# Optimization experiments

Hardware: AMD Instinct MI355X
Metric: run time of the kernel (lower is better)

## Reference

```python
import jax, jax.numpy as jnp
import numpy as np
import math

B, S, D, H, NB = 32, 512, 512, 8, 2
DK = D // H
DF = 4 * D
EPS = 1e-8


def layer_norm(x, gamma, beta):
    # Matches torch: unbiased std (ddof=1), divide by (std + eps)
    mean = jnp.mean(x, axis=-1, keepdims=True)
    std = jnp.sqrt(jnp.var(x, axis=-1, keepdims=True, ddof=1))
    return gamma * (x - mean) / (std + EPS) + beta


def block(x, wq, bq, wk, bk, wv, bv, wr, br, ga, ba, wc1, bc1, wc2, bc2, gf, bf):
    # --- attention with ReLU-gated Q/K/V ---
    Q = jax.nn.relu(x @ wq.T + bq)  # [B,S,D]
    K = jax.nn.relu(x @ wk.T + bk)
    V = jax.nn.relu(x @ wv.T + bv)
    # chunk along last dim -> heads; head-major stacking is equivalent to this reshape
    Qh = Q.reshape(B, S, H, DK)
    Kh = K.reshape(B, S, H, DK)
    Vh = V.reshape(B, S, H, DK)
    scores = jnp.einsum('bqhd,bkhd->bhqk', Qh, Kh) / math.sqrt(DK)
    w = jax.nn.softmax(scores, axis=-1)
    out = jnp.einsum('bhqk,bkhd->bqhd', w, Vh).reshape(B, S, D)
    out = out + jax.nn.relu(x @ wr.T + br)
    out = layer_norm(out, ga, ba)
    # --- conv1d (kernel=1) feed-forward ---
    h = jax.nn.relu(out @ wc1.T + bc1)  # [B,S,4D]
    y = h @ wc2.T + bc2                 # [B,S,D]
    y = layer_norm(y + out, gf, bf)
    return y


def setup_inputs() -> dict:
    key = jax.random.key(0)
    ks = jax.random.split(key, 8)
    std = 0.01
    inp = {
        'x': jax.random.normal(ks[0], (B, S, D), jnp.float32),
        'wq': jax.random.normal(ks[1], (NB, D, D), jnp.float32) * std,
        'bq': jnp.zeros((NB, D), jnp.float32),
        'wk': jax.random.normal(ks[2], (NB, D, D), jnp.float32) * std,
        'bk': jnp.zeros((NB, D), jnp.float32),
        'wv': jax.random.normal(ks[3], (NB, D, D), jnp.float32) * std,
        'bv': jnp.zeros((NB, D), jnp.float32),
        'wr': jax.random.normal(ks[4], (NB, D, D), jnp.float32) * std,
        'br': jnp.zeros((NB, D), jnp.float32),
        'g_attn': jnp.ones((NB, D), jnp.float32),
        'b_attn': jnp.zeros((NB, D), jnp.float32),
        'wc1': jax.random.normal(ks[5], (NB, DF, D), jnp.float32) * (1.0 / math.sqrt(D)),
        'bc1': jnp.zeros((NB, DF), jnp.float32),
        'wc2': jax.random.normal(ks[6], (NB, D, DF), jnp.float32) * (1.0 / math.sqrt(DF)),
        'bc2': jnp.zeros((NB, D), jnp.float32),
        'g_ffn': jnp.ones((NB, D), jnp.float32),
        'b_ffn': jnp.zeros((NB, D), jnp.float32),
    }
    return inp


def reference(x, wq, bq, wk, bk, wv, bv, wr, br, g_attn, b_attn,
              wc1, bc1, wc2, bc2, g_ffn, b_ffn):
    enc = x
    for i in range(NB):
        enc = block(enc, wq[i], bq[i], wk[i], bk[i], wv[i], bv[i], wr[i], br[i],
                    g_attn[i], b_attn[i], wc1[i], bc1[i], wc2[i], bc2[i],
                    g_ffn[i], b_ffn[i])
    return enc
```

## Files before the change

kernel.cpp:

```cpp
#include <hip/hip_runtime.h>

typedef unsigned short u16;
typedef __bf16 bf16x8 __attribute__((ext_vector_type(8)));
typedef float f32x4 __attribute__((ext_vector_type(4)));
typedef unsigned short ushort8 __attribute__((ext_vector_type(8)));

__device__ __forceinline__ void gload_lds16(const void* g, void* l) {
  __builtin_amdgcn_global_load_lds(
      (const __attribute__((address_space(1))) void*)g,
      (__attribute__((address_space(3))) void*)l, 16, 0, 0);
}

__device__ __forceinline__ u16 f2bf(float f) {
  unsigned int u = __builtin_bit_cast(unsigned int, f);
  u = (u + 0x7fffu + ((u >> 16) & 1u)) >> 16;
  return (u16)u;
}
__device__ __forceinline__ u16 f2bf_trunc(float f) {
  return (u16)(__builtin_bit_cast(unsigned int, f) >> 16);
}
__device__ __forceinline__ float bf2f(u16 u) {
  unsigned int v = (unsigned int)u << 16;
  return __builtin_bit_cast(float, v);
}

__global__ void castk(const float* __restrict__ in, u16* __restrict__ out, int n,
                      float scale) {
  size_t i = ((size_t)blockIdx.x * 256 + threadIdx.x) * 8;
  if (i >= (size_t)n) return;
  const float4* p = (const float4*)(in + i);
  float4 a = p[0], b = p[1];
  ushort8 o;
  o[0] = f2bf(a.x * scale); o[1] = f2bf(a.y * scale);
  o[2] = f2bf(a.z * scale); o[3] = f2bf(a.w * scale);
  o[4] = f2bf(b.x * scale); o[5] = f2bf(b.y * scale);
  o[6] = f2bf(b.z * scale); o[7] = f2bf(b.w * scale);
  *(ushort8*)(out + i) = o;
}

__global__ void biasg(const float* __restrict__ b0, const float* __restrict__ b1,
                      const float* __restrict__ b2, const float* __restrict__ b3,
                      float* __restrict__ out) {
  int idx = blockIdx.x * 256 + threadIdx.x;
  int i = idx >> 11, j = (idx >> 9) & 3, c = idx & 511;
  const float* src = (j == 0) ? b0 : (j == 1) ? b1 : (j == 2) ? b2 : b3;
  float v = src[i * 512 + c];
  out[idx] = (j == 0) ? v * 0.125f : v;
}

template<int BN, int RELU, int WVT>
__global__ __launch_bounds__(512, 4)
void gemm128(const u16* __restrict__ A, const u16* __restrict__ W,
             const float* __restrict__ bias, u16* __restrict__ C,
             u16* __restrict__ VT, int M, int N, int K)
{
  constexpr int CN   = BN / 4;
  constexpr int NF   = CN / 16;
  constexpr int ATSZ = 128 * 64;
  constexpr int BTSZ = BN * 64;
  constexpr int BLB  = BN / 128;
  constexpr int VC   = 1 + BLB;
  constexpr int PSZ  = 3 * (ATSZ + BTSZ);
  constexpr int ESZ  = 128 * BN * 2;
  constexpr int LSZ  = (PSZ > ESZ) ? PSZ : ESZ;

  __shared__ char lds[LSZ];

  const int tid = threadIdx.x, w = tid >> 6, l = tid & 63;
  const int l15 = l & 15, lh = l >> 4;
  const int nbn = N / BN;
  const int p = blockIdx.x;
  const int bm = (p & 7) * 16 + (p >> 3) / nbn;
  const int bn = (p >> 3) % nbn;
  const int wm = w >> 2, wn = w & 3;
  const int NT = K >> 5;

  const int srow = l >> 2;
  const int scol = ((l & 3) ^ ((l >> 3) & 3)) << 3;
  const u16* aS = A + (size_t)(bm * 128 + w * 16 + srow) * K + scol;
  const u16* bS[BLB];
#pragma unroll
  for (int j = 0; j < BLB; ++j)
    bS[j] = W + (size_t)(bn * BN + (w * BLB + j) * 16 + srow) * K + scol;

  auto stage = [&](int t) {
    const int bsel = t % 3;
    gload_lds16(aS + t * 32, lds + bsel * (ATSZ + BTSZ) + w * 1024);
#pragma unroll
    for (int j = 0; j < BLB; ++j)
      gload_lds16(bS[j] + t * 32,
                  lds + bsel * (ATSZ + BTSZ) + ATSZ + (w * BLB + j) * 1024);
  };

  f32x4 acc[4][NF] = {};
  const int sw = ((l15 >> 1) & 3) << 4;

  stage(0); stage(1);
  for (int u = 0; u < NT; ++u) {
    if (u + 1 < NT) asm volatile("s_waitcnt vmcnt(%0)" :: "i"(VC) : "memory");
    else            asm volatile("s_waitcnt vmcnt(0)" ::: "memory");
    __builtin_amdgcn_s_barrier();
    __builtin_amdgcn_sched_barrier(0);
    if (u + 2 < NT) stage(u + 2);

    const char* Ab = lds + (u % 3) * (ATSZ + BTSZ);
    const char* Bb = Ab + ATSZ;
    bf16x8 a[4], b[NF];
#pragma unroll
    for (int mf = 0; mf < 4; ++mf) {
      int row = wm * 64 + mf * 16 + l15;
      a[mf] = *(const bf16x8*)(Ab + row * 64 + ((lh << 4) ^ sw));
    }
#pragma unroll
    for (int nf = 0; nf < NF; ++nf) {
      int row = wn * CN + nf * 16 + l15;
      b[nf] = *(const bf16x8*)(Bb + row * 64 + ((lh << 4) ^ sw));
    }
    __builtin_amdgcn_s_setprio(1);
#pragma unroll
    for (int mf = 0; mf < 4; ++mf)
#pragma unroll
      for (int nf = 0; nf < NF; ++nf)
        acc[mf][nf] = __builtin_amdgcn_mfma_f32_16x16x32_bf16(a[mf], b[nf], acc[mf][nf], 0, 0, 0);
    __builtin_amdgcn_s_setprio(0);
  }

  __syncthreads();
  char* Ct = (char*)lds;
  const int rowL = wm * 64 + (lh << 2);
  const int colL = wn * CN + l15;
  const bool dovt = WVT && (bn == 4 || bn == 5);
  float bv[NF];
#pragma unroll
  for (int nf = 0; nf < NF; ++nf) bv[nf] = bias[bn * BN + colL + nf * 16];

  if (!dovt) {
#pragma unroll
    for (int mf = 0; mf < 4; ++mf)
#pragma unroll
      for (int nf = 0; nf < NF; ++nf)
#pragma unroll
        for (int r = 0; r < 4; ++r) {
          float v = acc[mf][nf][r] + bv[nf];
          if (RELU) v = fmaxf(v, 0.f);
          int m = rowL + mf * 16 + r, n = colL + nf * 16;
          *(u16*)(Ct + m * (BN * 2) + ((n * 2) ^ ((m & 7) << 4))) = f2bf(v);
        }
    __syncthreads();
    constexpr int TPR = (BN * 2) / 16;
    constexpr int RPP = 512 / TPR;
#pragma unroll
    for (int pass = 0; pass < 128 / RPP; ++pass) {
      int row = pass * RPP + tid / TPR;
      int c16 = tid % TPR;
      bf16x8 vv = *(const bf16x8*)(Ct + row * (BN * 2) + ((c16 * 16) ^ ((row & 7) << 4)));
      *(bf16x8*)(&C[(size_t)(bm * 128 + row) * N + bn * BN + c16 * 8]) = vv;
    }
  } else {
#pragma unroll
    for (int mf = 0; mf < 4; ++mf)
#pragma unroll
      for (int nf = 0; nf < NF; ++nf)
#pragma unroll
        for (int r = 0; r < 4; ++r) {
          float v = acc[mf][nf][r] + bv[nf];
          if (RELU) v = fmaxf(v, 0.f);
          int m = rowL + mf * 16 + r, d = colL + nf * 16;
          *(u16*)(Ct + d * 256 + ((m * 2) ^ ((d & 7) << 4))) = f2bf(v);
        }
    __syncthreads();
    const int batch = bm >> 2;
#pragma unroll
    for (int pass = 0; pass < 8; ++pass) {
      int dL = pass * 32 + (tid >> 4);
      int m16 = tid & 15;
      bf16x8 vv = *(const bf16x8*)(Ct + dL * 256 + ((m16 * 16) ^ ((dL & 7) << 4)));
      int head = (bn - 4) * 4 + (dL >> 6);
      int vtr = (batch * 8 + head) * 64 + (dL & 63);
      *(bf16x8*)(&VT[(size_t)vtr * 512 + (bm & 3) * 128 + m16 * 8]) = vv;
    }
  }
}

__global__ __launch_bounds__(256, 2)
void attn_kernel(const u16* __restrict__ qkvr, const u16* __restrict__ VT,
                 u16* __restrict__ F)
{
  const int D4 = 2048;
  __shared__ u16 Qs[128 * 64];
  __shared__ u16 Ks[2][64 * 64];
  __shared__ u16 Vs[2][64 * 64];
  __shared__ u16 Ps[128 * 64];

  const int tid = threadIdx.x, w = tid >> 6, l = tid & 63;
  const int bh = blockIdx.x & 255, qt = blockIdx.x >> 8;
  const int b = bh >> 3, h = bh & 7;
  const int lr = l >> 3, lc = ((l & 7) ^ lr) << 3;
  const int l15 = l & 15, lh = l >> 4;

  const u16* qG = qkvr + (size_t)(b * 512 + qt * 128) * D4 + h * 64 + lc;
#pragma unroll
  for (int i = 0; i < 4; ++i) {
    int c = w * 4 + i;
    gload_lds16(qG + (size_t)(c * 8 + lr) * D4, &Qs[c * 512]);
  }

  const u16* kG = qkvr + (size_t)(b * 512) * D4 + 512 + h * 64 + lc;
  const u16* vG = VT + (size_t)(bh * 64) * 512 + lc;

  auto stageKV = [&](int kt) {
    const int bsel = kt & 1;
#pragma unroll
    for (int i = 0; i < 2; ++i) {
      int c = w * 2 + i;
      gload_lds16(kG + (size_t)(kt * 64 + c * 8 + lr) * D4, &Ks[bsel][c * 512]);
      gload_lds16(vG + (size_t)(c * 8 + lr) * 512 + kt * 64, &Vs[bsel][c * 512]);
    }
  };
  stageKV(0);

  f32x4 o_acc[2][4] = {};
  float psum[2][4] = {};

  for (int kt = 0; kt < 8; ++kt) {
    __syncthreads();
    if (kt < 7) stageKV(kt + 1);
    const char* Kb = (const char*)Ks[kt & 1];
    const char* Vb = (const char*)Vs[kt & 1];

    f32x4 sacc[2][4] = {};
#pragma unroll
    for (int kk = 0; kk < 2; ++kk) {
      bf16x8 qa[2];
#pragma unroll
      for (int qq = 0; qq < 2; ++qq) {
        int qrow = w * 32 + qq * 16 + l15;
        qa[qq] = *(const bf16x8*)((const char*)Qs + qrow * 128 +
                  ((kk * 64 + (lh << 4)) ^ ((qrow & 7) << 4)));
      }
#pragma unroll
      for (int ni = 0; ni < 4; ++ni) {
        int krow = ni * 16 + l15;
        bf16x8 kb = *(const bf16x8*)(Kb + krow * 128 +
                    ((kk * 64 + (lh << 4)) ^ ((krow & 7) << 4)));
#pragma unroll
        for (int qq = 0; qq < 2; ++qq)
          sacc[qq][ni] = __builtin_amdgcn_mfma_f32_16x16x32_bf16(qa[qq], kb, sacc[qq][ni], 0, 0, 0);
      }
    }

#pragma unroll
    for (int qq = 0; qq < 2; ++qq)
#pragma unroll
      for (int r = 0; r < 4; ++r) {
        float p0 = __expf(sacc[qq][0][r]);
        float p1 = __expf(sacc[qq][1][r]);
        float p2 = __expf(sacc[qq][2][r]);
        float p3 = __expf(sacc[qq][3][r]);
        psum[qq][r] += (p0 + p1) + (p2 + p3);
        int q = w * 32 + qq * 16 + (lh << 2) + r;
        int sw = (q & 7) << 4;
        int col = l15 * 2;
        char* pb = (char*)Ps + q * 128;
        *(u16*)(pb + ((0  + col) ^ sw)) = f2bf_trunc(p0);
        *(u16*)(pb + ((32 + col) ^ sw)) = f2bf_trunc(p1);
        *(u16*)(pb + ((64 + col) ^ sw)) = f2bf_trunc(p2);
        *(u16*)(pb + ((96 + col) ^ sw)) = f2bf_trunc(p3);
      }

#pragma unroll
    for (int kk = 0; kk < 2; ++kk) {
      bf16x8 pa[2];
#pragma unroll
      for (int qq = 0; qq < 2; ++qq) {
        int qrow = w * 32 + qq * 16 + l15;
        pa[qq] = *(const bf16x8*)((const char*)Ps + qrow * 128 +
                  ((kk * 64 + (lh << 4)) ^ ((qrow & 7) << 4)));
      }
#pragma unroll
      for (int ni = 0; ni < 4; ++ni) {
        int d = ni * 16 + l15;
        bf16x8 vb = *(const bf16x8*)(Vb + d * 128 +
                    ((kk * 64 + (lh << 4)) ^ ((d & 7) << 4)));
#pragma unroll
        for (int qq = 0; qq < 2; ++qq)
          o_acc[qq][ni] = __builtin_amdgcn_mfma_f32_16x16x32_bf16(pa[qq], vb, o_acc[qq][ni], 0, 0, 0);
      }
    }
  }

  float lsum[2][4];
#pragma unroll
  for (int qq = 0; qq < 2; ++qq)
#pragma unroll
    for (int r = 0; r < 4; ++r) {
      float t = psum[qq][r];
#pragma unroll
      for (int m = 1; m < 16; m <<= 1) t += __shfl_xor(t, m);
      lsum[qq][r] = 1.f / t;
    }

#pragma unroll
  for (int qq = 0; qq < 2; ++qq)
#pragma unroll
    for (int ni = 0; ni < 4; ++ni) {
      int d = ni * 16 + l15;
#pragma unroll
      for (int r = 0; r < 4; ++r) {
        float v = o_acc[qq][ni][r] * lsum[qq][r];
        int q = w * 32 + qq * 16 + (lh << 2) + r;
        *(u16*)((char*)Ps + q * 128 + ((d * 2) ^ ((q & 7) << 4))) = f2bf(v);
      }
    }
  __syncthreads();
  const u16* Rbase = qkvr + (size_t)(b * 512 + qt * 128) * D4 + 1536 + h * 64;
  u16* Fbase = F + (size_t)(b * 512 + qt * 128) * 512 + h * 64;
#pragma unroll
  for (int pass = 0; pass < 4; ++pass) {
    int row = pass * 32 + (tid >> 3), c8 = tid & 7;
    ushort8 lv = *(const ushort8*)((char*)Ps + row * 128 + ((c8 * 16) ^ ((row & 7) << 4)));
    ushort8 rv = *(const ushort8*)(Rbase + (size_t)row * D4 + c8 * 8);
    ushort8 o;
#pragma unroll
    for (int j = 0; j < 8; ++j) o[j] = f2bf(bf2f(lv[j]) + bf2f(rv[j]));
    *(ushort8*)(Fbase + (size_t)row * 512 + c8 * 8) = o;
  }
}

template<int HAS_RES, int OUT_F32>
__global__ __launch_bounds__(256)
void ln_bf(const u16* __restrict__ in, const u16* __restrict__ res,
           const float* __restrict__ gamma, const float* __restrict__ beta,
           u16* __restrict__ outb, float* __restrict__ outf)
{
  const int l = threadIdx.x & 63;
  const size_t row = (size_t)blockIdx.x * 4 + (threadIdx.x >> 6);
  ushort8 iv = *(const ushort8*)(in + row * 512 + l * 8);
  float x[8];
#pragma unroll
  for (int j = 0; j < 8; ++j) x[j] = bf2f(iv[j]);
  if (HAS_RES) {
    ushort8 rv = *(const ushort8*)(res + row * 512 + l * 8);
#pragma unroll
    for (int j = 0; j < 8; ++j) x[j] += bf2f(rv[j]);
  }
  float s = 0.f, ss = 0.f;
#pragma unroll
  for (int j = 0; j < 8; ++j) { s += x[j]; ss += x[j] * x[j]; }
#pragma unroll
  for (int m = 1; m < 64; m <<= 1) { s += __shfl_xor(s, m); ss += __shfl_xor(ss, m); }
  float mean = s * (1.f / 512.f);
  float var = fmaxf((ss - 512.f * mean * mean) * (1.f / 511.f), 0.f);
  float inv = 1.f / (sqrtf(var) + 1e-8f);
  const float4* g4 = (const float4*)gamma;
  const float4* b4 = (const float4*)beta;
  float4 g0 = g4[l * 2], g1 = g4[l * 2 + 1];
  float4 b0 = b4[l * 2], b1 = b4[l * 2 + 1];
  float gg[8] = {g0.x, g0.y, g0.z, g0.w, g1.x, g1.y, g1.z, g1.w};
  float bb[8] = {b0.x, b0.y, b0.z, b0.w, b1.x, b1.y, b1.z, b1.w};
  float y[8];
#pragma unroll
  for (int j = 0; j < 8; ++j) y[j] = gg[j] * (x[j] - mean) * inv + bb[j];
  ushort8 o;
#pragma unroll
  for (int j = 0; j < 8; ++j) o[j] = f2bf(y[j]);
  *(ushort8*)(outb + row * 512 + l * 8) = o;
  if (OUT_F32) {
    float4* o4 = (float4*)(outf + row * 512);
    o4[l * 2]     = make_float4(y[0], y[1], y[2], y[3]);
    o4[l * 2 + 1] = make_float4(y[4], y[5], y[6], y[7]);
  }
}

extern "C" void kernel_launch(void* const* d_in, const int* in_sizes, int n_in,
                              void* d_out, int out_size, void* d_ws, size_t ws_size,
                              hipStream_t stream)
{
  const int B = 32, S = 512, D = 512, NB = 2, DF = 2048;
  const int M = B * S;

  const float* x   = (const float*)d_in[0];
  const float* wsrc[4] = {(const float*)d_in[1], (const float*)d_in[3],
                          (const float*)d_in[5], (const float*)d_in[7]};
  const float* ga  = (const float*)d_in[9];
  const float* ba  = (const float*)d_in[10];
  const float* wc1 = (const float*)d_in[11];
  const float* bc1 = (const float*)d_in[12];
  const float* wc2 = (const float*)d_in[13];
  const float* bc2 = (const float*)d_in[14];
  const float* gf  = (const float*)d_in[15];
  const float* bfp = (const float*)d_in[16];

  char* ws = (char*)d_ws;
  u16*   curb = (u16*)(ws + 0);
  u16*   qkvr = (u16*)(ws + 16777216);
  u16*   F    = (u16*)(ws + 83886080);
  u16*   Hg   = (u16*)(ws + 100663296);
  u16*   VT   = (u16*)(ws + 117440512);
  u16*   w4b  = (u16*)(ws + 134217728);
  u16*   wc1b = (u16*)(ws + 138412032);
  u16*   wc2b = (u16*)(ws + 142606336);
  float* b4   = (float*)(ws + 146800640);
  u16*   Ih   = qkvr;
  u16*   Y    = F;

  castk<<<M * D / 2048, 256, 0, stream>>>(x, curb, M * D, 1.0f);
  for (int i = 0; i < NB; ++i)
    for (int j = 0; j < 4; ++j)
      castk<<<128, 256, 0, stream>>>(wsrc[j] + (size_t)i * 262144,
                                     w4b + (size_t)i * 1048576 + j * 262144, 262144,
                                     (j == 0) ? 0.125f : 1.0f);
  biasg<<<16, 256, 0, stream>>>((const float*)d_in[2], (const float*)d_in[4],
                                (const float*)d_in[6], (const float*)d_in[8], b4);
  castk<<<NB * DF * D / 2048, 256, 0, stream>>>(wc1, wc1b, NB * DF * D, 1.0f);
  castk<<<NB * DF * D / 2048, 256, 0, stream>>>(wc2, wc2b, NB * DF * D, 1.0f);

  for (int i = 0; i < NB; ++i) {
    const size_t wfo = (size_t)i * DF * D;
    gemm128<256, 1, 1><<<1024, 512, 0, stream>>>(curb, w4b + (size_t)i * 1048576,
                                                 b4 + i * 2048, qkvr, VT, M, 2048, 512);
    attn_kernel<<<4 * 256, 256, 0, stream>>>(qkvr, VT, F);
    ln_bf<0, 0><<<M / 4, 256, 0, stream>>>(F, nullptr, ga + i * D, ba + i * D, Hg, nullptr);
    gemm128<256, 1, 0><<<1024, 512, 0, stream>>>(Hg, wc1b + wfo, bc1 + i * DF,
                                                 Ih, nullptr, M, 2048, 512);
    gemm128<128, 0, 0><<<512, 512, 0, stream>>>(Ih, wc2b + wfo, bc2 + i * D,
                                                Y, nullptr, M, 512, 2048);
    if (i == NB - 1)
      ln_bf<1, 1><<<M / 4, 256, 0, stream>>>(Y, Hg, gf + i * D, bfp + i * D,
                                             curb, (float*)d_out);
    else
      ln_bf<1, 0><<<M / 4, 256, 0, stream>>>(Y, Hg, gf + i * D, bfp + i * D,
                                             curb, nullptr);
  }
}
```

Measured before the change: 394.0 us.

## Load GEMM weight operand directly into registers, bypassing LDS

The GEMM kernel no longer stages the weight (B) tile through LDS. Each wave loads its B fragments straight from global memory into double-buffered registers one k-step ahead, while the activation (A) tile keeps an LDS ring, now four deep. The goal is to cut LDS traffic and capacity per block and remove the LDS reads of B. In exchange, waves that share B columns fetch the same data separately through L2, and the vmcnt(1) wait also forces the A prefetch issued in the same step to finish early, which shortens the effective pipelining depth. Separately, the eight per-matrix weight-cast launches are merged into a single castw4 kernel.

New measurement: 590.6 us. 49.9% more time.

```diff
diff --git a/kernel.cpp b/kernel.cpp
--- a/kernel.cpp
+++ b/kernel.cpp
@@ -38,6 +38,25 @@
   *(ushort8*)(out + i) = o;
 }
 
+__global__ void castw4(const float* __restrict__ w0, const float* __restrict__ w1,
+                       const float* __restrict__ w2, const float* __restrict__ w3,
+                       u16* __restrict__ out) {
+  size_t idx = ((size_t)blockIdx.x * 256 + threadIdx.x) * 8;
+  int i = (int)(idx >> 20);
+  int j = (int)((idx >> 18) & 3);
+  int e = (int)(idx & 262143);
+  const float* src = (j == 0) ? w0 : (j == 1) ? w1 : (j == 2) ? w2 : w3;
+  float scale = (j == 0) ? 0.125f : 1.0f;
+  const float4* p = (const float4*)(src + (size_t)i * 262144 + e);
+  float4 a = p[0], b = p[1];
+  ushort8 o;
+  o[0] = f2bf(a.x * scale); o[1] = f2bf(a.y * scale);
+  o[2] = f2bf(a.z * scale); o[3] = f2bf(a.w * scale);
+  o[4] = f2bf(b.x * scale); o[5] = f2bf(b.y * scale);
+  o[6] = f2bf(b.z * scale); o[7] = f2bf(b.w * scale);
+  *(ushort8*)(out + idx) = o;
+}
+
 __global__ void biasg(const float* __restrict__ b0, const float* __restrict__ b1,
                       const float* __restrict__ b2, const float* __restrict__ b3,
                       float* __restrict__ out) {
@@ -50,17 +69,14 @@
 
 template<int BN, int RELU, int WVT>
 __global__ __launch_bounds__(512, 4)
-void gemm128(const u16* __restrict__ A, const u16* __restrict__ W,
-             const float* __restrict__ bias, u16* __restrict__ C,
-             u16* __restrict__ VT, int M, int N, int K)
+void gemmBD(const u16* __restrict__ A, const u16* __restrict__ W,
+            const float* __restrict__ bias, u16* __restrict__ C,
+            u16* __restrict__ VT, int M, int N, int K)
 {
   constexpr int CN   = BN / 4;
   constexpr int NF   = CN / 16;
   constexpr int ATSZ = 128 * 64;
-  constexpr int BTSZ = BN * 64;
-  constexpr int BLB  = BN / 128;
-  constexpr int VC   = 1 + BLB;
-  constexpr int PSZ  = 3 * (ATSZ + BTSZ);
+  constexpr int PSZ  = 4 * ATSZ;
   constexpr int ESZ  = 128 * BN * 2;
   constexpr int LSZ  = (PSZ > ESZ) ? PSZ : ESZ;
 
@@ -78,51 +94,54 @@
   const int srow = l >> 2;
   const int scol = ((l & 3) ^ ((l >> 3) & 3)) << 3;
   const u16* aS = A + (size_t)(bm * 128 + w * 16 + srow) * K + scol;
-  const u16* bS[BLB];
-#pragma unroll
-  for (int j = 0; j < BLB; ++j)
-    bS[j] = W + (size_t)(bn * BN + (w * BLB + j) * 16 + srow) * K + scol;
-
-  auto stage = [&](int t) {
-    const int bsel = t % 3;
-    gload_lds16(aS + t * 32, lds + bsel * (ATSZ + BTSZ) + w * 1024);
-#pragma unroll
-    for (int j = 0; j < BLB; ++j)
-      gload_lds16(bS[j] + t * 32,
-                  lds + bsel * (ATSZ + BTSZ) + ATSZ + (w * BLB + j) * 1024);
+  auto stageA = [&](int t) {
+    gload_lds16(aS + t * 32, lds + (t & 3) * ATSZ + w * 1024);
   };
+
+  const u16* bG = W + (size_t)(bn * BN + wn * CN + l15) * K + lh * 8;
 
   f32x4 acc[4][NF] = {};
   const int sw = ((l15 >> 1) & 3) << 4;
-
-  stage(0); stage(1);
-  for (int u = 0; u < NT; ++u) {
-    if (u + 1 < NT) asm volatile("s_waitcnt vmcnt(%0)" :: "i"(VC) : "memory");
+  bf16x8 bP[NF], bQ[NF];
+
+  stageA(0);
+#pragma unroll
+  for (int nf = 0; nf < NF; ++nf)
+    bP[nf] = *(const bf16x8*)(bG + (size_t)nf * 16 * K);
+  stageA(1);
+
+  auto body = [&](int t, bf16x8 (&bc)[NF], bf16x8 (&bnx)[NF], int bufsel) {
+    if (t + 1 < NT) asm volatile("s_waitcnt vmcnt(1)" ::: "memory");
     else            asm volatile("s_waitcnt vmcnt(0)" ::: "memory");
     __builtin_amdgcn_s_barrier();
     __builtin_amdgcn_sched_barrier(0);
-    if (u + 2 < NT) stage(u + 2);
-
-    const char* Ab = lds + (u % 3) * (ATSZ + BTSZ);
-    const char* Bb = Ab + ATSZ;
-    bf16x8 a[4], b[NF];
+    if (t + 2 < NT) stageA(t + 2);
+    if (t + 1 < NT) {
+#pragma unroll
+      for (int nf = 0; nf < NF; ++nf)
+        bnx[nf] = *(const bf16x8*)(bG + (size_t)nf * 16 * K + (t + 1) * 32);
+    }
+    const char* Ab = lds + bufsel * ATSZ;
+    bf16x8 a[4];
 #pragma unroll
     for (int mf = 0; mf < 4; ++mf) {
       int row = wm * 64 + mf * 16 + l15;
       a[mf] = *(const bf16x8*)(Ab + row * 64 + ((lh << 4) ^ sw));
     }
-#pragma unroll
-    for (int nf = 0; nf < NF; ++nf) {
-      int row = wn * CN + nf * 16 + l15;
-      b[nf] = *(const bf16x8*)(Bb + row * 64 + ((lh << 4) ^ sw));
-    }
     __builtin_amdgcn_s_setprio(1);
 #pragma unroll
     for (int mf = 0; mf < 4; ++mf)
 #pragma unroll
       for (int nf = 0; nf < NF; ++nf)
-        acc[mf][nf] = __builtin_amdgcn_mfma_f32_16x16x32_bf16(a[mf], b[nf], acc[mf][nf], 0, 0, 0);
+        acc[mf][nf] = __builtin_amdgcn_mfma_f32_16x16x32_bf16(a[mf], bc[nf], acc[mf][nf], 0, 0, 0);
     __builtin_amdgcn_s_setprio(0);
+  };
+
+  for (int u = 0; u < NT; u += 4) {
+    body(u,     bP, bQ, 0);
+    body(u + 1, bQ, bP, 1);
+    body(u + 2, bP, bQ, 2);
+    body(u + 3, bQ, bP, 3);
   }
 
   __syncthreads();
@@ -380,8 +399,6 @@
   const int M = B * S;
 
   const float* x   = (const float*)d_in[0];
-  const float* wsrc[4] = {(const float*)d_in[1], (const float*)d_in[3],
-                          (const float*)d_in[5], (const float*)d_in[7]};
   const float* ga  = (const float*)d_in[9];
   const float* ba  = (const float*)d_in[10];
   const float* wc1 = (const float*)d_in[11];
@@ -405,11 +422,8 @@
   u16*   Y    = F;
 
   castk<<<M * D / 2048, 256, 0, stream>>>(x, curb, M * D, 1.0f);
-  for (int i = 0; i < NB; ++i)
-    for (int j = 0; j < 4; ++j)
-      castk<<<128, 256, 0, stream>>>(wsrc[j] + (size_t)i * 262144,
-                                     w4b + (size_t)i * 1048576 + j * 262144, 262144,
-                                     (j == 0) ? 0.125f : 1.0f);
+  castw4<<<1024, 256, 0, stream>>>((const float*)d_in[1], (const float*)d_in[3],
+                                   (const float*)d_in[5], (const float*)d_in[7], w4b);
   biasg<<<16, 256, 0, stream>>>((const float*)d_in[2], (const float*)d_in[4],
                                 (const float*)d_in[6], (const float*)d_in[8], b4);
   castk<<<NB * DF * D / 2048, 256, 0, stream>>>(wc1, wc1b, NB * DF * D, 1.0f);
@@ -417,14 +431,14 @@
 
   for (int i = 0; i < NB; ++i) {
     const size_t wfo = (size_t)i * DF * D;
-    gemm128<256, 1, 1><<<1024, 512, 0, stream>>>(curb, w4b + (size_t)i * 1048576,
-                                                 b4 + i * 2048, qkvr, VT, M, 2048, 512);
+    gemmBD<256, 1, 1><<<1024, 512, 0, stream>>>(curb, w4b + (size_t)i * 1048576,
+                                                b4 + i * 2048, qkvr, VT, M, 2048, 512);
     attn_kernel<<<4 * 256, 256, 0, stream>>>(qkvr, VT, F);
     ln_bf<0, 0><<<M / 4, 256, 0, stream>>>(F, nullptr, ga + i * D, ba + i * D, Hg, nullptr);
-    gemm128<256, 1, 0><<<1024, 512, 0, stream>>>(Hg, wc1b + wfo, bc1 + i * DF,
-                                                 Ih, nullptr, M, 2048, 512);
-    gemm128<128, 0, 0><<<512, 512, 0, stream>>>(Ih, wc2b + wfo, bc2 + i * D,
-                                                Y, nullptr, M, 512, 2048);
+    gemmBD<256, 1, 0><<<1024, 512, 0, stream>>>(Hg, wc1b + wfo, bc1 + i * DF,
+                                                Ih, nullptr, M, 2048, 512);
+    gemmBD<128, 0, 0><<<512, 512, 0, stream>>>(Ih, wc2b + wfo, bc2 + i * D,
+                                               Y, nullptr, M, 512, 2048);
     if (i == NB - 1)
       ln_bf<1, 1><<<M / 4, 256, 0, stream>>>(Y, Hg, gf + i * D, bfp + i * D,
                                              curb, (float*)d_out);
```
